# Kernel tuning notes

Measured on AMD Instinct MI355X. Metric: run time of the kernel, lower is better.

The kernel has to match this reference:

```python
import jax, jax.numpy as jnp
import numpy as np

ALPHA = 1.0  # module hardcodes self.alpha = 1.0


def _normalize(m):
    # torch: diag(rowsum^-0.5) @ m @ diag(rowsum^-0.5) == broadcast row/col scaling
    r_inv = jnp.sum(m, axis=0) ** -0.5  # [V]
    return m * r_inv[:, None] * r_inv[None, :]


def setup_inputs() -> dict:
    key = jax.random.key(0)
    k1, k2, k3, k4 = jax.random.split(key, 4)
    V, D_IN, D_OUT, A, B = 2048, 64, 64, 8, 8
    adj = jax.random.uniform(k1, (V, V), dtype=jnp.float32)
    x = jax.random.normal(k2, (A, B, V, D_IN), dtype=jnp.float32)
    # xavier_normal_ on [D_IN, D_OUT]
    std = float(np.sqrt(2.0 / (D_IN + D_OUT)))
    weight = jax.random.normal(k3, (D_IN, D_OUT), dtype=jnp.float32) * std
    bias = jax.random.normal(k4, (D_OUT,), dtype=jnp.float32)
    return {"adj": adj, "x": x, "weight": weight, "bias": bias}


def reference(adj, x, weight, bias):
    # dropout is identity in eval mode
    adj_norm = _normalize(adj)
    sqr_norm = _normalize(adj @ adj)  # computed as in the original (alpha=1 zeroes it)
    m_norm = ALPHA * adj_norm + (1.0 - ALPHA) * sqr_norm  # [V, V]
    x_tmp = jnp.einsum('abvd,de->abve', x, weight)        # project features
    x_out = jnp.einsum('vj,abvd->abjd', m_norm, x_tmp)    # aggregate over nodes
    x_out = x_out + bias
    return jax.nn.relu(x_out)
```

## Files before the change

### kernel.cpp

```cpp
#include <hip/hip_runtime.h>
#include <cstddef>

typedef unsigned short u16;
typedef u16 u16x8 __attribute__((ext_vector_type(8)));
typedef __bf16 bf16x8 __attribute__((ext_vector_type(8)));
typedef float f32x4 __attribute__((ext_vector_type(4)));

static constexpr int V  = 2048;
static constexpr int DD = 64;

__device__ __forceinline__ u16 f2b(float f) {
  union { float f; unsigned int i; } x; x.f = f;
  return (u16)((x.i + 0x7fffu + ((x.i >> 16) & 1u)) >> 16);
}

__device__ __forceinline__ void gll16(const void* g, void* l) {
  __builtin_amdgcn_global_load_lds(
      (const __attribute__((address_space(1))) void*)g,
      (__attribute__((address_space(3))) void*)l, 16, 0, 0);
}

__global__ __launch_bounds__(256) void k_part(const float* __restrict__ adj,
                                              float* __restrict__ partial) {
  int t = threadIdx.x;
  int r0 = blockIdx.x * 16;
  int c0 = t * 8;
  float acc[8] = {0.f, 0.f, 0.f, 0.f, 0.f, 0.f, 0.f, 0.f};
  for (int r = 0; r < 16; ++r) {
    const float4* p = (const float4*)(adj + (size_t)(r0 + r) * V + c0);
    float4 a0 = p[0], a1 = p[1];
    acc[0] += a0.x; acc[1] += a0.y; acc[2] += a0.z; acc[3] += a0.w;
    acc[4] += a1.x; acc[5] += a1.y; acc[6] += a1.z; acc[7] += a1.w;
  }
  #pragma unroll
  for (int k = 0; k < 8; ++k) partial[(size_t)blockIdx.x * V + c0 + k] = acc[k];
}

__global__ __launch_bounds__(256) void k_rinv(const float* __restrict__ partial,
                                              float* __restrict__ rinv) {
  int c = blockIdx.x * 256 + threadIdx.x;
  float s = 0.f;
  for (int i = 0; i < 128; ++i) s += partial[(size_t)i * V + c];
  rinv[c] = rsqrtf(s);
}

__global__ __launch_bounds__(256) void k_tn(const float* __restrict__ adj,
                                            const float* __restrict__ rinv,
                                            u16* __restrict__ At) {
  __shared__ float T[64][65];
  int t = threadIdx.x;
  int v0 = blockIdx.x * 64;
  int j0 = blockIdx.y * 64;
  #pragma unroll
  for (int it = 0; it < 2; ++it) {
    int f = t + it * 256;
    int row = f >> 3;
    int cc = (f & 7) * 8;
    float rv = rinv[v0 + row];
    const float4* p = (const float4*)(adj + (size_t)(v0 + row) * V + j0 + cc);
    float4 a0 = p[0], a1 = p[1];
    T[row][cc + 0] = a0.x * rv; T[row][cc + 1] = a0.y * rv;
    T[row][cc + 2] = a0.z * rv; T[row][cc + 3] = a0.w * rv;
    T[row][cc + 4] = a1.x * rv; T[row][cc + 5] = a1.y * rv;
    T[row][cc + 6] = a1.z * rv; T[row][cc + 7] = a1.w * rv;
  }
  __syncthreads();
  #pragma unroll
  for (int it = 0; it < 2; ++it) {
    int f = t + it * 256;
    int jr = f >> 3;
    int vc = (f & 7) * 8;
    float rj = rinv[j0 + jr];
    u16x8 o;
    #pragma unroll
    for (int k = 0; k < 8; ++k) o[k] = f2b(T[vc + k][jr] * rj);
    *(u16x8*)(At + (size_t)(j0 + jr) * V + v0 + vc) = o;
  }
}

__global__ __launch_bounds__(256) void k_proj(const float* __restrict__ x,
                                              const float* __restrict__ w,
                                              u16* __restrict__ Yt) {
  __shared__ u16 WT[64 * 72];
  int t = threadIdx.x;
  int ab = blockIdx.x >> 4;
  int v0 = (blockIdx.x & 15) * 128;

  {
    const float4* pw = (const float4*)(w + t * 16);
    float4 c0 = pw[0], c1 = pw[1], c2 = pw[2], c3 = pw[3];
    float vals[16] = {c0.x, c0.y, c0.z, c0.w, c1.x, c1.y, c1.z, c1.w,
                      c2.x, c2.y, c2.z, c2.w, c3.x, c3.y, c3.z, c3.w};
    #pragma unroll
    for (int k = 0; k < 16; ++k) {
      int idx = t * 16 + k;
      WT[(idx & 63) * 72 + (idx >> 6)] = f2b(vals[k]);
    }
  }
  __syncthreads();

  int lane = t & 63, wave = t >> 6;
  int q = lane >> 4, r = lane & 15;
  int vbase = v0 + wave * 32;

  bf16x8 a[4][2];
  #pragma unroll
  for (int i = 0; i < 4; ++i)
    #pragma unroll
    for (int kk = 0; kk < 2; ++kk)
      a[i][kk] = __builtin_bit_cast(bf16x8,
          *(const u16x8*)(WT + (i * 16 + r) * 72 + kk * 32 + q * 8));

  const f32x4 vzero = {0.f, 0.f, 0.f, 0.f};
  f32x4 acc[4][2];
  #pragma unroll
  for (int i = 0; i < 4; ++i) { acc[i][0] = vzero; acc[i][1] = vzero; }

  #pragma unroll
  for (int nt = 0; nt < 2; ++nt) {
    int v = vbase + nt * 16 + r;
    const float* xp = x + ((size_t)ab * V + v) * DD;
    #pragma unroll
    for (int kk = 0; kk < 2; ++kk) {
      const float4* p = (const float4*)(xp + kk * 32 + q * 8);
      float4 b0 = p[0], b1 = p[1];
      u16x8 bu;
      bu[0] = f2b(b0.x); bu[1] = f2b(b0.y); bu[2] = f2b(b0.z); bu[3] = f2b(b0.w);
      bu[4] = f2b(b1.x); bu[5] = f2b(b1.y); bu[6] = f2b(b1.z); bu[7] = f2b(b1.w);
      bf16x8 bf = __builtin_bit_cast(bf16x8, bu);
      #pragma unroll
      for (int i = 0; i < 4; ++i)
        acc[i][nt] = __builtin_amdgcn_mfma_f32_16x16x32_bf16(a[i][kk], bf, acc[i][nt], 0, 0, 0);
    }
  }

  #pragma unroll
  for (int i = 0; i < 4; ++i)
    #pragma unroll
    for (int nt = 0; nt < 2; ++nt) {
      int v = vbase + nt * 16 + r;
      #pragma unroll
      for (int reg = 0; reg < 4; ++reg) {
        int e = i * 16 + q * 4 + reg;
        Yt[(size_t)(ab * 64 + e) * V + v] = f2b(acc[i][nt][reg]);
      }
    }
}

#define BM 128
#define BN 128
#define PANEL (128 * 32)

__global__ __launch_bounds__(256) void k_gemm(const u16* __restrict__ At,
                                              const u16* __restrict__ Yt,
                                              const float* __restrict__ bias,
                                              float* __restrict__ out) {
  __shared__ u16 Al[4 * PANEL];
  __shared__ u16 Bl[4 * PANEL];
  int t = threadIdx.x;
  int m0 = blockIdx.x * BM;
  int n0 = blockIdx.y * BN;
  int lane = t & 63;
  int wave = t >> 6;
  int wm = (wave & 1) * 64;
  int wn = (wave >> 1) * 64;
  int q = lane >> 4;
  int r = lane & 15;

  const f32x4 vzero = {0.f, 0.f, 0.f, 0.f};
  f32x4 acc[4][4];
  #pragma unroll
  for (int i = 0; i < 4; ++i)
    #pragma unroll
    for (int j = 0; j < 4; ++j) acc[i][j] = vzero;

  int eo0 = t * 8;
  int eo1 = (256 + t) * 8;
  int row0 = eo0 >> 5, col0 = eo0 & 31;
  int row1 = eo1 >> 5, col1 = eo1 & 31;

  for (int k0 = 0; k0 < V; k0 += 128) {
    __syncthreads();
    #pragma unroll
    for (int p = 0; p < 4; ++p) {
      int kp = k0 + p * 32;
      gll16(At + (size_t)(m0 + row0) * V + kp + col0, Al + p * PANEL + eo0);
      gll16(At + (size_t)(m0 + row1) * V + kp + col1, Al + p * PANEL + eo1);
      gll16(Yt + (size_t)(n0 + row0) * V + kp + col0, Bl + p * PANEL + eo0);
      gll16(Yt + (size_t)(n0 + row1) * V + kp + col1, Bl + p * PANEL + eo1);
    }
    __syncthreads();
    #pragma unroll
    for (int p = 0; p < 4; ++p) {
      bf16x8 a[4], b[4];
      #pragma unroll
      for (int i = 0; i < 4; ++i)
        a[i] = __builtin_bit_cast(bf16x8,
            *(const u16x8*)(Al + p * PANEL + (wm + i * 16 + r) * 32 + q * 8));
      #pragma unroll
      for (int j = 0; j < 4; ++j)
        b[j] = __builtin_bit_cast(bf16x8,
            *(const u16x8*)(Bl + p * PANEL + (wn + j * 16 + r) * 32 + q * 8));
      #pragma unroll
      for (int i = 0; i < 4; ++i)
        #pragma unroll
        for (int j = 0; j < 4; ++j)
          acc[i][j] = __builtin_amdgcn_mfma_f32_16x16x32_bf16(a[i], b[j], acc[i][j], 0, 0, 0);
    }
  }

  #pragma unroll
  for (int j = 0; j < 4; ++j) {
    int n = n0 + wn + j * 16 + r;
    int e = n & 63;
    int ab = n >> 6;
    float bv = bias[e];
    float* ob = out + (size_t)ab * (V * DD);
    #pragma unroll
    for (int i = 0; i < 4; ++i) {
      #pragma unroll
      for (int reg = 0; reg < 4; ++reg) {
        int jj = m0 + wm + i * 16 + q * 4 + reg;
        ob[(size_t)jj * DD + e] = fmaxf(acc[i][j][reg] + bv, 0.f);
      }
    }
  }
}

extern "C" void kernel_launch(void* const* d_in, const int* in_sizes, int n_in,
                              void* d_out, int out_size, void* d_ws, size_t ws_size,
                              hipStream_t stream) {
  const float* adj  = (const float*)d_in[0];
  const float* x    = (const float*)d_in[1];
  const float* w    = (const float*)d_in[2];
  const float* bias = (const float*)d_in[3];
  float* out = (float*)d_out;

  char* ws = (char*)d_ws;
  u16*   At      = (u16*)ws;
  u16*   Yt      = (u16*)(ws + ((size_t)8 << 20));
  float* partial = (float*)(ws + ((size_t)8 << 20));
  float* rinv    = (float*)(ws + ((size_t)9 << 20));

  k_part<<<128, 256, 0, stream>>>(adj, partial);
  k_rinv<<<8, 256, 0, stream>>>(partial, rinv);
  k_tn<<<dim3(32, 32), 256, 0, stream>>>(adj, rinv, At);
  k_proj<<<1024, 256, 0, stream>>>(x, w, Yt);
  k_gemm<<<dim3(16, 32), 256, 0, stream>>>(At, Yt, bias, out);
}
```

Before: 153.7 us.

## Fuse rinv, transpose-normalize and projection kernels into one prep launch

Merges the rinv reduction into the transpose kernel, where each block recomputes the scales for its 64 rows and 64 columns from the partial sums. It also runs the projection kernel as extra blocks of the same launch, so the two independent stages can overlap and launch overhead drops from five kernels to three. The column-sum kernel now covers 32 rows per block, halving the partial buffer to 64 rows. In exchange, each transpose block repeats some of the column-sum reduction work.

Result: faster. 148.8 us (median of 2 runs) (-3.2%).

```diff
diff --git a/kernel.cpp b/kernel.cpp
--- a/kernel.cpp
+++ b/kernel.cpp
@@ -23,10 +23,10 @@
 __global__ __launch_bounds__(256) void k_part(const float* __restrict__ adj,
                                               float* __restrict__ partial) {
   int t = threadIdx.x;
-  int r0 = blockIdx.x * 16;
+  int r0 = blockIdx.x * 32;
   int c0 = t * 8;
   float acc[8] = {0.f, 0.f, 0.f, 0.f, 0.f, 0.f, 0.f, 0.f};
-  for (int r = 0; r < 16; ++r) {
+  for (int r = 0; r < 32; ++r) {
     const float4* p = (const float4*)(adj + (size_t)(r0 + r) * V + c0);
     float4 a0 = p[0], a1 = p[1];
     acc[0] += a0.x; acc[1] += a0.y; acc[2] += a0.z; acc[3] += a0.w;
@@ -36,115 +36,119 @@
   for (int k = 0; k < 8; ++k) partial[(size_t)blockIdx.x * V + c0 + k] = acc[k];
 }
 
-__global__ __launch_bounds__(256) void k_rinv(const float* __restrict__ partial,
-                                              float* __restrict__ rinv) {
-  int c = blockIdx.x * 256 + threadIdx.x;
-  float s = 0.f;
-  for (int i = 0; i < 128; ++i) s += partial[(size_t)i * V + c];
-  rinv[c] = rsqrtf(s);
-}
-
-__global__ __launch_bounds__(256) void k_tn(const float* __restrict__ adj,
-                                            const float* __restrict__ rinv,
-                                            u16* __restrict__ At) {
+__global__ __launch_bounds__(256) void k_prep(const float* __restrict__ adj,
+                                              const float* __restrict__ partial,
+                                              const float* __restrict__ x,
+                                              const float* __restrict__ w,
+                                              u16* __restrict__ At,
+                                              u16* __restrict__ Yt) {
   __shared__ float T[64][65];
+  __shared__ float rvv[64], rvj[64];
   int t = threadIdx.x;
-  int v0 = blockIdx.x * 64;
-  int j0 = blockIdx.y * 64;
-  #pragma unroll
-  for (int it = 0; it < 2; ++it) {
-    int f = t + it * 256;
-    int row = f >> 3;
-    int cc = (f & 7) * 8;
-    float rv = rinv[v0 + row];
-    const float4* p = (const float4*)(adj + (size_t)(v0 + row) * V + j0 + cc);
-    float4 a0 = p[0], a1 = p[1];
-    T[row][cc + 0] = a0.x * rv; T[row][cc + 1] = a0.y * rv;
-    T[row][cc + 2] = a0.z * rv; T[row][cc + 3] = a0.w * rv;
-    T[row][cc + 4] = a1.x * rv; T[row][cc + 5] = a1.y * rv;
-    T[row][cc + 6] = a1.z * rv; T[row][cc + 7] = a1.w * rv;
-  }
-  __syncthreads();
-  #pragma unroll
-  for (int it = 0; it < 2; ++it) {
-    int f = t + it * 256;
-    int jr = f >> 3;
-    int vc = (f & 7) * 8;
-    float rj = rinv[j0 + jr];
-    u16x8 o;
-    #pragma unroll
-    for (int k = 0; k < 8; ++k) o[k] = f2b(T[vc + k][jr] * rj);
-    *(u16x8*)(At + (size_t)(j0 + jr) * V + v0 + vc) = o;
-  }
-}
-
-__global__ __launch_bounds__(256) void k_proj(const float* __restrict__ x,
-                                              const float* __restrict__ w,
-                                              u16* __restrict__ Yt) {
-  __shared__ u16 WT[64 * 72];
-  int t = threadIdx.x;
-  int ab = blockIdx.x >> 4;
-  int v0 = (blockIdx.x & 15) * 128;
-
-  {
-    const float4* pw = (const float4*)(w + t * 16);
-    float4 c0 = pw[0], c1 = pw[1], c2 = pw[2], c3 = pw[3];
-    float vals[16] = {c0.x, c0.y, c0.z, c0.w, c1.x, c1.y, c1.z, c1.w,
-                      c2.x, c2.y, c2.z, c2.w, c3.x, c3.y, c3.z, c3.w};
-    #pragma unroll
-    for (int k = 0; k < 16; ++k) {
-      int idx = t * 16 + k;
-      WT[(idx & 63) * 72 + (idx >> 6)] = f2b(vals[k]);
-    }
-  }
-  __syncthreads();
-
-  int lane = t & 63, wave = t >> 6;
-  int q = lane >> 4, r = lane & 15;
-  int vbase = v0 + wave * 32;
-
-  bf16x8 a[4][2];
-  #pragma unroll
-  for (int i = 0; i < 4; ++i)
-    #pragma unroll
-    for (int kk = 0; kk < 2; ++kk)
-      a[i][kk] = __builtin_bit_cast(bf16x8,
-          *(const u16x8*)(WT + (i * 16 + r) * 72 + kk * 32 + q * 8));
-
-  const f32x4 vzero = {0.f, 0.f, 0.f, 0.f};
-  f32x4 acc[4][2];
-  #pragma unroll
-  for (int i = 0; i < 4; ++i) { acc[i][0] = vzero; acc[i][1] = vzero; }
-
-  #pragma unroll
-  for (int nt = 0; nt < 2; ++nt) {
-    int v = vbase + nt * 16 + r;
-    const float* xp = x + ((size_t)ab * V + v) * DD;
-    #pragma unroll
-    for (int kk = 0; kk < 2; ++kk) {
-      const float4* p = (const float4*)(xp + kk * 32 + q * 8);
-      float4 b0 = p[0], b1 = p[1];
-      u16x8 bu;
-      bu[0] = f2b(b0.x); bu[1] = f2b(b0.y); bu[2] = f2b(b0.z); bu[3] = f2b(b0.w);
-      bu[4] = f2b(b1.x); bu[5] = f2b(b1.y); bu[6] = f2b(b1.z); bu[7] = f2b(b1.w);
-      bf16x8 bf = __builtin_bit_cast(bf16x8, bu);
-      #pragma unroll
-      for (int i = 0; i < 4; ++i)
-        acc[i][nt] = __builtin_amdgcn_mfma_f32_16x16x32_bf16(a[i][kk], bf, acc[i][nt], 0, 0, 0);
-    }
-  }
-
-  #pragma unroll
-  for (int i = 0; i < 4; ++i)
+  int bid = blockIdx.x;
+
+  if (bid < 1024) {
+    int v0 = (bid & 31) * 64;
+    int j0 = (bid >> 5) * 64;
+    if (t < 128) {
+      int col = (t < 64) ? (v0 + t) : (j0 + (t - 64));
+      float s = 0.f;
+      for (int i = 0; i < 64; ++i) s += partial[(size_t)i * V + col];
+      float rv = rsqrtf(s);
+      if (t < 64) rvv[t] = rv; else rvj[t - 64] = rv;
+    }
+    __syncthreads();
+    #pragma unroll
+    for (int it = 0; it < 2; ++it) {
+      int f = t + it * 256;
+      int row = f >> 3;
+      int cc = (f & 7) * 8;
+      float rv = rvv[row];
+      const float4* p = (const float4*)(adj + (size_t)(v0 + row) * V + j0 + cc);
+      float4 a0 = p[0], a1 = p[1];
+      T[row][cc + 0] = a0.x * rv; T[row][cc + 1] = a0.y * rv;
+      T[row][cc + 2] = a0.z * rv; T[row][cc + 3] = a0.w * rv;
+      T[row][cc + 4] = a1.x * rv; T[row][cc + 5] = a1.y * rv;
+      T[row][cc + 6] = a1.z * rv; T[row][cc + 7] = a1.w * rv;
+    }
+    __syncthreads();
+    #pragma unroll
+    for (int it = 0; it < 2; ++it) {
+      int f = t + it * 256;
+      int jr = f >> 3;
+      int vc = (f & 7) * 8;
+      float rj = rvj[jr];
+      u16x8 o;
+      #pragma unroll
+      for (int k = 0; k < 8; ++k) o[k] = f2b(T[vc + k][jr] * rj);
+      *(u16x8*)(At + (size_t)(j0 + jr) * V + v0 + vc) = o;
+    }
+  } else {
+    int pb = bid - 1024;
+    int ab = pb >> 4;
+    int v0 = (pb & 15) * 128;
+    u16* WT = (u16*)&T[0][0];
+
+    {
+      const float4* pw = (const float4*)(w + t * 16);
+      float4 c0 = pw[0], c1 = pw[1], c2 = pw[2], c3 = pw[3];
+      float vals[16] = {c0.x, c0.y, c0.z, c0.w, c1.x, c1.y, c1.z, c1.w,
+                        c2.x, c2.y, c2.z, c2.w, c3.x, c3.y, c3.z, c3.w};
+      #pragma unroll
+      for (int k = 0; k < 16; ++k) {
+        int idx = t * 16 + k;
+        WT[(idx & 63) * 72 + (idx >> 6)] = f2b(vals[k]);
+      }
+    }
+    __syncthreads();
+
+    int lane = t & 63, wave = t >> 6;
+    int q = lane >> 4, r = lane & 15;
+    int vbase = v0 + wave * 32;
+
+    bf16x8 a[4][2];
+    #pragma unroll
+    for (int i = 0; i < 4; ++i)
+      #pragma unroll
+      for (int kk = 0; kk < 2; ++kk)
+        a[i][kk] = __builtin_bit_cast(bf16x8,
+            *(const u16x8*)(WT + (i * 16 + r) * 72 + kk * 32 + q * 8));
+
+    const f32x4 vzero = {0.f, 0.f, 0.f, 0.f};
+    f32x4 acc[4][2];
+    #pragma unroll
+    for (int i = 0; i < 4; ++i) { acc[i][0] = vzero; acc[i][1] = vzero; }
+
     #pragma unroll
     for (int nt = 0; nt < 2; ++nt) {
       int v = vbase + nt * 16 + r;
-      #pragma unroll
-      for (int reg = 0; reg < 4; ++reg) {
-        int e = i * 16 + q * 4 + reg;
-        Yt[(size_t)(ab * 64 + e) * V + v] = f2b(acc[i][nt][reg]);
-      }
-    }
+      const float* xp = x + ((size_t)ab * V + v) * DD;
+      #pragma unroll
+      for (int kk = 0; kk < 2; ++kk) {
+        const float4* p = (const float4*)(xp + kk * 32 + q * 8);
+        float4 b0 = p[0], b1 = p[1];
+        u16x8 bu;
+        bu[0] = f2b(b0.x); bu[1] = f2b(b0.y); bu[2] = f2b(b0.z); bu[3] = f2b(b0.w);
+        bu[4] = f2b(b1.x); bu[5] = f2b(b1.y); bu[6] = f2b(b1.z); bu[7] = f2b(b1.w);
+        bf16x8 bf = __builtin_bit_cast(bf16x8, bu);
+        #pragma unroll
+        for (int i = 0; i < 4; ++i)
+          acc[i][nt] = __builtin_amdgcn_mfma_f32_16x16x32_bf16(a[i][kk], bf, acc[i][nt], 0, 0, 0);
+      }
+    }
+
+    #pragma unroll
+    for (int i = 0; i < 4; ++i)
+      #pragma unroll
+      for (int nt = 0; nt < 2; ++nt) {
+        int v = vbase + nt * 16 + r;
+        #pragma unroll
+        for (int reg = 0; reg < 4; ++reg) {
+          int e = i * 16 + q * 4 + reg;
+          Yt[(size_t)(ab * 64 + e) * V + v] = f2b(acc[i][nt][reg]);
+        }
+      }
+  }
 }
 
 #define BM 128
@@ -239,12 +243,9 @@
   char* ws = (char*)d_ws;
   u16*   At      = (u16*)ws;
   u16*   Yt      = (u16*)(ws + ((size_t)8 << 20));
-  float* partial = (float*)(ws + ((size_t)8 << 20));
-  float* rinv    = (float*)(ws + ((size_t)9 << 20));
-
-  k_part<<<128, 256, 0, stream>>>(adj, partial);
-  k_rinv<<<8, 256, 0, stream>>>(partial, rinv);
-  k_tn<<<dim3(32, 32), 256, 0, stream>>>(adj, rinv, At);
-  k_proj<<<1024, 256, 0, stream>>>(x, w, Yt);
+  float* partial = (float*)(ws + ((size_t)24 << 20));
+
+  k_part<<<64, 256, 0, stream>>>(adj, partial);
+  k_prep<<<2048, 256, 0, stream>>>(adj, partial, x, w, At, Yt);
   k_gemm<<<dim3(16, 32), 256, 0, stream>>>(At, Yt, bias, out);
 }
```
